# Kernel tuning notes

Hardware: AMD Instinct MI355X
Metric: run time of the kernel (lower is better)

Reference implementation:

```python
import jax, jax.numpy as jnp
import numpy as np

N = 100000      # nodes
E = 1250000     # edges
DIN = 128       # input_feature_dim
H = 64          # hidden_feature_dim
C = 16          # num_classes
BN_EPS = 1e-5


def _linear_init(key, fin, fout):
    # torch.nn.Linear default: U(-1/sqrt(fin), 1/sqrt(fin)); stored as [fin, fout] for x @ W
    s = 1.0 / np.sqrt(fin)
    kw, kb = jax.random.split(key)
    w = jax.random.uniform(kw, (fin, fout), jnp.float32, -s, s)
    b = jax.random.uniform(kb, (fout,), jnp.float32, -s, s)
    return w, b


def setup_inputs() -> dict:
    key = jax.random.key(0)
    ks = jax.random.split(key, 16)
    inp = {}
    inp["x"] = jax.random.normal(ks[0], (N, DIN), jnp.float32)
    src = jax.random.randint(ks[1], (E,), 0, N)
    dst = jax.random.randint(ks[2], (E,), 0, N)
    inp["edge_index"] = jnp.stack([src, dst]).astype(jnp.int64)
    inp["fc1_w"], inp["fc1_b"] = _linear_init(ks[3], DIN, H)
    dims = [(H, H), (H, H), (H, C)]
    for i, (fi, fo) in enumerate(dims):
        w, b = _linear_init(ks[4 + i], fi, fo)
        inp[f"conv{i}_w"] = w
        inp[f"conv{i}_b"] = b
        inp[f"bn{i}_g"] = jnp.ones((fo,), jnp.float32)
        inp[f"bn{i}_b"] = jnp.zeros((fo,), jnp.float32)
    inp["fc2_w"], inp["fc2_b"] = _linear_init(ks[7], C, C)
    return inp


def gcn_conv(h, w, b, src, dst, n):
    # PyG GCNConv: linear transform, add self-loops, symmetric normalization,
    # scatter-add messages from src into dst, then add bias.
    h = h @ w                                   # [N, out]
    loops = jnp.arange(n)
    s = jnp.concatenate([src, loops])           # [E+N]
    d = jnp.concatenate([dst, loops])
    deg = jax.ops.segment_sum(jnp.ones(s.shape[0], h.dtype), d, num_segments=n)
    dinv = jnp.where(deg > 0, jax.lax.rsqrt(deg), 0.0)
    norm = dinv[s] * dinv[d]                    # [E+N]
    msg = h[s] * norm[:, None]                  # [E+N, out] gather + scale
    out = jax.ops.segment_sum(msg, d, num_segments=n)
    return out + b


def batch_norm(x, gamma, beta):
    # BatchNorm1d in training mode: biased batch statistics over nodes
    mu = x.mean(axis=0)
    var = x.var(axis=0)
    return (x - mu) * jax.lax.rsqrt(var + BN_EPS) * gamma + beta


def reference(x, edge_index, fc1_w, fc1_b,
              conv0_w, conv0_b, bn0_g, bn0_b,
              conv1_w, conv1_b, bn1_g, bn1_b,
              conv2_w, conv2_b, bn2_g, bn2_b,
              fc2_w, fc2_b):
    src, dst = edge_index[0], edge_index[1]
    n = x.shape[0]
    h = jax.nn.relu(x @ fc1_w + fc1_b)
    layers = [(conv0_w, conv0_b, bn0_g, bn0_b),
              (conv1_w, conv1_b, bn1_g, bn1_b),
              (conv2_w, conv2_b, bn2_g, bn2_b)]
    for w, b, g, be in layers:
        h = jax.nn.relu(batch_norm(gcn_conv(h, w, b, src, dst, n), g, be))
    h = h @ fc2_w + fc2_b
    return jax.nn.log_softmax(h, axis=1)
```

## Files before the change

kernel.cpp:

```cpp
#include <hip/hip_runtime.h>

#define BN_EPS 1e-5f

typedef unsigned int uint32;

__device__ __forceinline__ void fma4(float4& a, float s, const float4& w) {
    a.x = fmaf(s, w.x, a.x); a.y = fmaf(s, w.y, a.y);
    a.z = fmaf(s, w.z, a.z); a.w = fmaf(s, w.w, a.w);
}

__device__ __forceinline__ float blo(uint32 p) { return __uint_as_float(p << 16); }
__device__ __forceinline__ float bhi(uint32 p) { return __uint_as_float(p & 0xFFFF0000u); }
__device__ __forceinline__ uint32 f2bf1(float f) {
    uint32 u = __float_as_uint(f);
    return (u + 0x7FFFu + ((u >> 16) & 1u)) >> 16;
}
__device__ __forceinline__ uint32 packbf(float a, float b) { return f2bf1(a) | (f2bf1(b) << 16); }


__global__ __launch_bounds__(256) void k_scan1(const int* __restrict__ deg, int* __restrict__ off,
                                               int* __restrict__ bsum, float* __restrict__ dinv, int n) {
    __shared__ int sh[256];
    int i = blockIdx.x * 256 + threadIdx.x;
    int v = (i < n) ? deg[i] : 0;
    if (i < n) dinv[i] = rsqrtf((float)v + 1.0f);
    sh[threadIdx.x] = v;
    __syncthreads();
    #pragma unroll
    for (int d = 1; d < 256; d <<= 1) {
        int t = (threadIdx.x >= d) ? sh[threadIdx.x - d] : 0;
        __syncthreads();
        sh[threadIdx.x] += t;
        __syncthreads();
    }
    if (i < n) off[i] = sh[threadIdx.x] - v;
    if (threadIdx.x == 255) bsum[blockIdx.x] = sh[255];
}

__global__ __launch_bounds__(512) void k_scan2(int* bsum, int nb) {
    __shared__ int sh[512];
    int v = (threadIdx.x < nb) ? bsum[threadIdx.x] : 0;
    sh[threadIdx.x] = v;
    __syncthreads();
    #pragma unroll
    for (int d = 1; d < 512; d <<= 1) {
        int t = (threadIdx.x >= d) ? sh[threadIdx.x - d] : 0;
        __syncthreads();
        sh[threadIdx.x] += t;
        __syncthreads();
    }
    if (threadIdx.x < nb) bsum[threadIdx.x] = sh[threadIdx.x] - v;
}

__global__ __launch_bounds__(256) void k_scan3(int* __restrict__ off, const int* __restrict__ bsum,
                                               int* __restrict__ cnt, int n, int e) {
    int i = blockIdx.x * 256 + threadIdx.x;
    if (i < n) { off[i] += bsum[blockIdx.x]; cnt[i] = 0; }
    if (i == 0) off[n] = e;
}


__global__ __launch_bounds__(256) void k_fc1_deg(const float* __restrict__ X, const float* __restrict__ W,
                                                 const float* __restrict__ bias, float* __restrict__ Y,
                                                 const int* __restrict__ dst, int* __restrict__ deg,
                                                 int n, int e, int nbLin) {
    constexpr int FIN = 128, FOUT = 64, KC = 64;
    constexpr int TX = FOUT / 4, TY = 256 / TX, RQ = 8, TILE_R = TY * RQ;
    __shared__ float Xs[TILE_R][KC + 4];
    __shared__ float Ws[KC][FOUT + 4];

    const int bid = blockIdx.x;
    const int twice = 2 * nbLin;
    bool isLin; int vid;
    if (bid < twice) { isLin = ((bid & 1) == 0); vid = bid >> 1; }
    else { isLin = false; vid = nbLin + (bid - twice); }

    if (!isLin) {
        const int ndeg = gridDim.x - nbLin;
        for (size_t i = (size_t)vid * 256 + threadIdx.x; i < (size_t)e; i += (size_t)ndeg * 256)
            atomicAdd(&deg[dst[i]], 1);
        return;
    }

    const int tx = threadIdx.x % TX;
    const int ty = threadIdx.x / TX;
    const float4 bb = *(const float4*)(bias + tx * 4);

    for (int r0 = vid * TILE_R; r0 < n; r0 += nbLin * TILE_R) {
        float4 acc[RQ];
        #pragma unroll
        for (int q = 0; q < RQ; ++q) acc[q] = bb;

        for (int kc = 0; kc < FIN; kc += KC) {
            __syncthreads();
            for (int idx = threadIdx.x; idx < TILE_R * (KC / 4); idx += 256) {
                int rr = idx / (KC / 4), k4 = idx % (KC / 4);
                int row = r0 + rr;
                float4 v = make_float4(0.f, 0.f, 0.f, 0.f);
                if (row < n) v = *(const float4*)(X + (size_t)row * FIN + kc + 4 * k4);
                *(float4*)(&Xs[rr][4 * k4]) = v;
            }
            for (int idx = threadIdx.x; idx < KC * (FOUT / 4); idx += 256) {
                int kk = idx / (FOUT / 4), c4 = idx % (FOUT / 4);
                *(float4*)(&Ws[kk][4 * c4]) = *(const float4*)(W + (size_t)(kc + kk) * FOUT + 4 * c4);
            }
            __syncthreads();

            #pragma unroll 4
            for (int k4 = 0; k4 < KC / 4; ++k4) {
                float4 w0 = *(const float4*)(&Ws[4*k4+0][tx*4]);
                float4 w1 = *(const float4*)(&Ws[4*k4+1][tx*4]);
                float4 w2 = *(const float4*)(&Ws[4*k4+2][tx*4]);
                float4 w3 = *(const float4*)(&Ws[4*k4+3][tx*4]);
                #pragma unroll
                for (int q = 0; q < RQ; ++q) {
                    float4 xv = *(const float4*)(&Xs[ty*RQ+q][4*k4]);
                    fma4(acc[q], xv.x, w0);
                    fma4(acc[q], xv.y, w1);
                    fma4(acc[q], xv.z, w2);
                    fma4(acc[q], xv.w, w3);
                }
            }
        }

        #pragma unroll
        for (int q = 0; q < RQ; ++q) {
            int row = r0 + ty * RQ + q;
            if (row < n) {
                float4 v = acc[q];
                v.x = fmaxf(v.x, 0.f); v.y = fmaxf(v.y, 0.f);
                v.z = fmaxf(v.z, 0.f); v.w = fmaxf(v.w, 0.f);
                *(float4*)(Y + (size_t)row * FOUT + tx * 4) = v;
            }
        }
    }
}


__global__ __launch_bounds__(256) void k_conv0_fill(const float* __restrict__ X, const float* __restrict__ W,
                                                    uint2* __restrict__ Yb, const float* __restrict__ dinv,
                                                    const int* __restrict__ src, const int* __restrict__ dst,
                                                    const int* __restrict__ off, int* __restrict__ cnt,
                                                    int* __restrict__ esrc, int n, int e, int nbLin) {
    constexpr int FIN = 64, FOUT = 64, KC = 64;
    constexpr int TX = FOUT / 4, TY = 256 / TX, RQ = 8, TILE_R = TY * RQ;
    __shared__ float Xs[TILE_R][KC + 4];
    __shared__ float Ws[KC][FOUT + 4];

    const int bid = blockIdx.x;
    const int twice = 2 * nbLin;
    bool isLin; int vid;
    if (bid < twice) { isLin = ((bid & 1) == 0); vid = bid >> 1; }
    else { isLin = false; vid = nbLin + (bid - twice); }

    if (!isLin) {
        const int nfl = gridDim.x - nbLin;
        for (size_t i = (size_t)vid * 256 + threadIdx.x; i < (size_t)e; i += (size_t)nfl * 256) {
            int d = dst[i];
            int slot = off[d] + atomicAdd(&cnt[d], 1);
            esrc[slot] = src[i];
        }
        return;
    }

    const int tx = threadIdx.x % TX;
    const int ty = threadIdx.x / TX;

    for (int r0 = vid * TILE_R; r0 < n; r0 += nbLin * TILE_R) {
        float4 acc[RQ];
        #pragma unroll
        for (int q = 0; q < RQ; ++q) acc[q] = make_float4(0.f, 0.f, 0.f, 0.f);

        __syncthreads();
        for (int idx = threadIdx.x; idx < TILE_R * (KC / 4); idx += 256) {
            int rr = idx / (KC / 4), k4 = idx % (KC / 4);
            int row = r0 + rr;
            float4 v = make_float4(0.f, 0.f, 0.f, 0.f);
            if (row < n) v = *(const float4*)(X + (size_t)row * FIN + 4 * k4);
            *(float4*)(&Xs[rr][4 * k4]) = v;
        }
        for (int idx = threadIdx.x; idx < KC * (FOUT / 4); idx += 256) {
            int kk = idx / (FOUT / 4), c4 = idx % (FOUT / 4);
            *(float4*)(&Ws[kk][4 * c4]) = *(const float4*)(W + (size_t)kk * FOUT + 4 * c4);
        }
        __syncthreads();

        #pragma unroll 4
        for (int k4 = 0; k4 < KC / 4; ++k4) {
            float4 w0 = *(const float4*)(&Ws[4*k4+0][tx*4]);
            float4 w1 = *(const float4*)(&Ws[4*k4+1][tx*4]);
            float4 w2 = *(const float4*)(&Ws[4*k4+2][tx*4]);
            float4 w3 = *(const float4*)(&Ws[4*k4+3][tx*4]);
            #pragma unroll
            for (int q = 0; q < RQ; ++q) {
                float4 xv = *(const float4*)(&Xs[ty*RQ+q][4*k4]);
                fma4(acc[q], xv.x, w0);
                fma4(acc[q], xv.y, w1);
                fma4(acc[q], xv.z, w2);
                fma4(acc[q], xv.w, w3);
            }
        }

        #pragma unroll
        for (int q = 0; q < RQ; ++q) {
            int row = r0 + ty * RQ + q;
            if (row < n) {
                float4 v = acc[q];
                float dv = dinv[row];
                v.x *= dv; v.y *= dv; v.z *= dv; v.w *= dv;
                uint2 pk;
                pk.x = packbf(v.x, v.y);
                pk.y = packbf(v.z, v.w);
                Yb[(size_t)row * (FOUT / 4) + tx] = pk;
            }
        }
    }
}


template<int FIN, int FOUT, bool RELU, bool BIAS, bool BNIN, bool DSCALE, bool OBF>
__global__ __launch_bounds__(256) void k_linear(const float* __restrict__ X, const float* __restrict__ W,
                                                const float* __restrict__ bias, void* __restrict__ Yv,
                                                const float* __restrict__ S, const float* __restrict__ bng,
                                                const float* __restrict__ bnb, const float* __restrict__ dinv,
                                                float inv_n, int n) {
    constexpr int KC = 64;
    constexpr int TX = FOUT / 4;
    constexpr int TY = 256 / TX;
    constexpr int RQ = (FOUT == 64) ? 8 : 2;
    constexpr int TILE_R = TY * RQ;
    constexpr int LDX = KC + 4;
    constexpr int LDW = FOUT + 4;
    __shared__ float Xs[TILE_R][LDX];
    __shared__ float Ws[KC][LDW];
    __shared__ float scs[BNIN ? FIN : 4], sfs[BNIN ? FIN : 4];

    const int tx = threadIdx.x % TX;
    const int ty = threadIdx.x / TX;

    if (BNIN) {
        for (int c = threadIdx.x; c < FIN; c += 256) {
            float mu = S[c] * inv_n;
            float var = S[FIN + c] * inv_n - mu * mu;
            float is = rsqrtf(var + BN_EPS) * bng[c];
            scs[c] = is;
            sfs[c] = bnb[c] - mu * is;
        }
        __syncthreads();
    }

    float4 bb = make_float4(0.f, 0.f, 0.f, 0.f);
    if (BIAS) bb = *(const float4*)(bias + tx * 4);

    for (int r0 = blockIdx.x * TILE_R; r0 < n; r0 += gridDim.x * TILE_R) {
        float4 acc[RQ];
        #pragma unroll
        for (int q = 0; q < RQ; ++q) acc[q] = bb;

        for (int kc = 0; kc < FIN; kc += KC) {
            __syncthreads();
            for (int idx = threadIdx.x; idx < TILE_R * (KC / 4); idx += 256) {
                int rr = idx / (KC / 4), k4 = idx % (KC / 4);
                int row = r0 + rr;
                float4 v = make_float4(0.f, 0.f, 0.f, 0.f);
                if (row < n) v = *(const float4*)(X + (size_t)row * FIN + kc + 4 * k4);
                if (BNIN) {
                    int c = kc + 4 * k4;
                    v.x = fmaxf(fmaf(v.x, scs[c+0], sfs[c+0]), 0.f);
                    v.y = fmaxf(fmaf(v.y, scs[c+1], sfs[c+1]), 0.f);
                    v.z = fmaxf(fmaf(v.z, scs[c+2], sfs[c+2]), 0.f);
                    v.w = fmaxf(fmaf(v.w, scs[c+3], sfs[c+3]), 0.f);
                }
                *(float4*)(&Xs[rr][4 * k4]) = v;
            }
            for (int idx = threadIdx.x; idx < KC * (FOUT / 4); idx += 256) {
                int kk = idx / (FOUT / 4), c4 = idx % (FOUT / 4);
                *(float4*)(&Ws[kk][4 * c4]) = *(const float4*)(W + (size_t)(kc + kk) * FOUT + 4 * c4);
            }
            __syncthreads();

            #pragma unroll 4
            for (int k4 = 0; k4 < KC / 4; ++k4) {
                float4 w0 = *(const float4*)(&Ws[4*k4+0][tx*4]);
                float4 w1 = *(const float4*)(&Ws[4*k4+1][tx*4]);
                float4 w2 = *(const float4*)(&Ws[4*k4+2][tx*4]);
                float4 w3 = *(const float4*)(&Ws[4*k4+3][tx*4]);
                #pragma unroll
                for (int q = 0; q < RQ; ++q) {
                    float4 xv = *(const float4*)(&Xs[ty*RQ+q][4*k4]);
                    fma4(acc[q], xv.x, w0);
                    fma4(acc[q], xv.y, w1);
                    fma4(acc[q], xv.z, w2);
                    fma4(acc[q], xv.w, w3);
                }
            }
        }

        #pragma unroll
        for (int q = 0; q < RQ; ++q) {
            int row = r0 + ty * RQ + q;
            if (row < n) {
                float4 v = acc[q];
                if (RELU) {
                    v.x = fmaxf(v.x, 0.f); v.y = fmaxf(v.y, 0.f);
                    v.z = fmaxf(v.z, 0.f); v.w = fmaxf(v.w, 0.f);
                }
                if (DSCALE) {
                    float dv = dinv[row];
                    v.x *= dv; v.y *= dv; v.z *= dv; v.w *= dv;
                }
                if (OBF) {
                    uint2 pk;
                    pk.x = packbf(v.x, v.y);
                    pk.y = packbf(v.z, v.w);
                    ((uint2*)Yv)[(size_t)row * (FOUT / 4) + tx] = pk;
                } else {
                    *(float4*)((float*)Yv + (size_t)row * FOUT + tx * 4) = v;
                }
            }
        }
    }
}


__global__ __launch_bounds__(256) void k_accum64bf(const uint32* __restrict__ Tb, const int* __restrict__ esrc,
                                                   const int* __restrict__ off, const float* __restrict__ dinv,
                                                   const float* __restrict__ bias, float* __restrict__ Z,
                                                   float* __restrict__ S, int n, int e) {
    __shared__ uint32 ring[4][2][256];
    __shared__ float sA[4][64], sB[4][64];

    const int lane = threadIdx.x & 63;
    const int wid  = threadIdx.x >> 6;
    const int rsub = lane >> 3;
    const int csub = lane & 7;
    const int cidx = lane >> 1;
    const int chal = lane & 1;
    const float bcol = bias[lane];

    float s1 = 0.f, s2 = 0.f;

    const int gw = blockIdx.x * 4 + wid;
    const int NW = gridDim.x * 4;
    const int eS = (int)((long long)gw * e / NW);
    const int eE = (int)((long long)(gw + 1) * e / NW);

    int lo = 0, hi = n;
    while (lo < hi) { int mid = (lo + hi) >> 1; if (off[mid] < eS) lo = mid + 1; else hi = mid; }
    const int d0 = lo;
    int d1;
    if (gw == NW - 1) d1 = n;
    else {
        lo = d0; hi = n;
        while (lo < hi) { int mid = (lo + hi) >> 1; if (off[mid] < eE) lo = mid + 1; else hi = mid; }
        d1 = lo;
    }

    if (d0 < d1) {
        const int e0 = off[d0];
        const int e1 = off[d1];
        const int nt = (e1 - e0 + 7) >> 3;

        uint32* slot0 = &ring[wid][0][0];
        uint32* slot1 = &ring[wid][1][0];

        int d = d0;
        int nxt = off[d + 1];
        uint32 selfp = Tb[(size_t)d * 32 + cidx];
        float  dv    = dinv[d];
        float  part  = 0.f;
        int    ec    = e0;

        auto tload = [&](int t) -> uint4 {
            int ei = min(e0 + t * 8 + rsub, e1 - 1);
            int s = esrc[ei];
            return ((const uint4*)Tb)[(size_t)s * 8 + csub];
        };

        uint4 B0, B1, B2;
        if (nt > 0) B0 = tload(0);
        if (nt > 1) B1 = tload(1);
        if (nt > 2) B2 = tload(2);

        for (int t = 0; t < nt; ++t) {
            uint32* sl = (t & 1) ? slot1 : slot0;
            uint4 cur = (t % 3 == 0) ? B0 : (t % 3 == 1) ? B1 : B2;
            *(uint4*)(sl + lane * 4) = cur;
            if (t + 3 < nt) {
                if (t % 3 == 0) B0 = tload(t + 3);
                else if (t % 3 == 1) B1 = tload(t + 3);
                else B2 = tload(t + 3);
            }
            int rend = min(8, e1 - (e0 + t * 8));
            for (int r = 0; r < rend; ++r) {
                while (ec == nxt) {
                    float sv = chal ? bhi(selfp) : blo(selfp);
                    float z = fmaf(part + sv, dv, bcol);
                    Z[(size_t)d * 64 + lane] = z;
                    s1 += z; s2 += z * z;
                    part = 0.f;
                    ++d;
                    nxt = off[d + 1];
                    selfp = Tb[(size_t)d * 32 + cidx];
                    dv = dinv[d];
                }
                uint32 p = sl[r * 32 + cidx];
                part += chal ? bhi(p) : blo(p);
                ++ec;
            }
        }
        while (d < d1) {
            float sv = chal ? bhi(selfp) : blo(selfp);
            float z = fmaf(part + sv, dv, bcol);
            Z[(size_t)d * 64 + lane] = z;
            s1 += z; s2 += z * z;
            part = 0.f;
            ++d;
            if (d < d1) {
                selfp = Tb[(size_t)d * 32 + cidx];
                dv = dinv[d];
            }
        }
    }

    sA[wid][lane] = s1;
    sB[wid][lane] = s2;
    __syncthreads();
    if (threadIdx.x < 64) {
        float t1 = 0.f, t2 = 0.f;
        #pragma unroll
        for (int w = 0; w < 4; ++w) { t1 += sA[w][threadIdx.x]; t2 += sB[w][threadIdx.x]; }
        atomicAdd(&S[threadIdx.x], t1);
        atomicAdd(&S[64 + threadIdx.x], t2);
    }
}


__global__ __launch_bounds__(256) void k_accum16bf(const uint2* __restrict__ Tb2, const int* __restrict__ esrc,
                                                   const int* __restrict__ off, const float* __restrict__ dinv,
                                                   const float* __restrict__ bias, float* __restrict__ Z,
                                                   float* __restrict__ S, int n) {
    const int lane = threadIdx.x & 63;
    const int wid  = threadIdx.x >> 6;
    const int lp   = lane & 3;
    const int es   = lane >> 2;
    const float4 bb = *(const float4*)(bias + 4 * lp);
    float st1[4] = {0.f,0.f,0.f,0.f}, st2[4] = {0.f,0.f,0.f,0.f};
    const uint2 z2 = make_uint2(0u, 0u);

    for (int dp = blockIdx.x * 4 + wid; 2 * dp < n; dp += gridDim.x * 4) {
        const int dA = 2 * dp, dB = 2 * dp + 1;
        const int oA0 = off[dA], oA1 = off[dA + 1];
        const int oB0 = oA1;
        const int oB1 = (dB < n) ? off[dB + 1] : oA1;

        float aA0=0.f, aA1=0.f, aA2=0.f, aA3=0.f;
        float aB0=0.f, aB1=0.f, aB2=0.f, aB3=0.f;
        int bA = oA0, bB = oB0;
        while (bA < oA1 || bB < oB1) {
            if (bA < oA1) {
                int i0 = bA + es;
                int s0 = (i0 < oA1) ? esrc[i0] : -1;
                uint2 p0 = (s0 >= 0) ? Tb2[(size_t)s0 * 4 + lp] : z2;
                aA0 += blo(p0.x); aA1 += bhi(p0.x); aA2 += blo(p0.y); aA3 += bhi(p0.y);
            }
            if (bB < oB1) {
                int i0 = bB + es;
                int s0 = (i0 < oB1) ? esrc[i0] : -1;
                uint2 p0 = (s0 >= 0) ? Tb2[(size_t)s0 * 4 + lp] : z2;
                aB0 += blo(p0.x); aB1 += bhi(p0.x); aB2 += blo(p0.y); aB3 += bhi(p0.y);
            }
            bA += 16; bB += 16;
        }

        #pragma unroll
        for (int sh = 4; sh <= 32; sh <<= 1) {
            aA0 += __shfl_xor(aA0, sh); aA1 += __shfl_xor(aA1, sh);
            aA2 += __shfl_xor(aA2, sh); aA3 += __shfl_xor(aA3, sh);
            aB0 += __shfl_xor(aB0, sh); aB1 += __shfl_xor(aB1, sh);
            aB2 += __shfl_xor(aB2, sh); aB3 += __shfl_xor(aB3, sh);
        }

        if (es == 0) {
            uint2 ps = Tb2[(size_t)dA * 4 + lp];
            float dv = dinv[dA];
            float4 zz;
            zz.x = fmaf(aA0 + blo(ps.x), dv, bb.x);
            zz.y = fmaf(aA1 + bhi(ps.x), dv, bb.y);
            zz.z = fmaf(aA2 + blo(ps.y), dv, bb.z);
            zz.w = fmaf(aA3 + bhi(ps.y), dv, bb.w);
            *(float4*)(Z + (size_t)dA * 16 + 4 * lp) = zz;
            st1[0] += zz.x; st2[0] += zz.x * zz.x;
            st1[1] += zz.y; st2[1] += zz.y * zz.y;
            st1[2] += zz.z; st2[2] += zz.z * zz.z;
            st1[3] += zz.w; st2[3] += zz.w * zz.w;
            if (dB < n) {
                uint2 pb = Tb2[(size_t)dB * 4 + lp];
                float dvB = dinv[dB];
                float4 zb;
                zb.x = fmaf(aB0 + blo(pb.x), dvB, bb.x);
                zb.y = fmaf(aB1 + bhi(pb.x), dvB, bb.y);
                zb.z = fmaf(aB2 + blo(pb.y), dvB, bb.z);
                zb.w = fmaf(aB3 + bhi(pb.y), dvB, bb.w);
                *(float4*)(Z + (size_t)dB * 16 + 4 * lp) = zb;
                st1[0] += zb.x; st2[0] += zb.x * zb.x;
                st1[1] += zb.y; st2[1] += zb.y * zb.y;
                st1[2] += zb.z; st2[2] += zb.z * zb.z;
                st1[3] += zb.w; st2[3] += zb.w * zb.w;
            }
        }
    }

    __shared__ float sh1[4][16], sh2[4][16];
    if (es == 0) {
        *(float4*)(&sh1[wid][4 * lp]) = make_float4(st1[0], st1[1], st1[2], st1[3]);
        *(float4*)(&sh2[wid][4 * lp]) = make_float4(st2[0], st2[1], st2[2], st2[3]);
    }
    __syncthreads();
    if (threadIdx.x < 16) {
        float t1 = 0.f, t2 = 0.f;
        #pragma unroll
        for (int w = 0; w < 4; ++w) { t1 += sh1[w][threadIdx.x]; t2 += sh2[w][threadIdx.x]; }
        atomicAdd(&S[threadIdx.x], t1);
        atomicAdd(&S[16 + threadIdx.x], t2);
    }
}


__global__ __launch_bounds__(256) void k_fc2_lsm(const float* __restrict__ Hin, const float* __restrict__ W,
                                                 const float* __restrict__ bias, const float* __restrict__ S,
                                                 const float* __restrict__ bng, const float* __restrict__ bnb,
                                                 float inv_n, float* __restrict__ out, int n) {
    __shared__ float Ws[256];
    __shared__ float bs[16], sc[16], sf[16];
    Ws[threadIdx.x] = W[threadIdx.x];
    if (threadIdx.x < 16) {
        int c = threadIdx.x;
        bs[c] = bias[c];
        float mu = S[c] * inv_n;
        float var = S[16 + c] * inv_n - mu * mu;
        float is = rsqrtf(var + BN_EPS) * bng[c];
        sc[c] = is;
        sf[c] = bnb[c] - mu * is;
    }
    __syncthreads();
    for (int row = blockIdx.x * 256 + threadIdx.x; row < n; row += gridDim.x * 256) {
        float h[16];
        const float4* hp = (const float4*)(Hin + (size_t)row * 16);
        #pragma unroll
        for (int q = 0; q < 4; ++q) {
            float4 h4 = hp[q];
            h[q*4+0] = h4.x; h[q*4+1] = h4.y; h[q*4+2] = h4.z; h[q*4+3] = h4.w;
        }
        #pragma unroll
        for (int k = 0; k < 16; ++k) h[k] = fmaxf(fmaf(h[k], sc[k], sf[k]), 0.0f);
        float o[16];
        #pragma unroll
        for (int c = 0; c < 16; ++c) {
            float acc = bs[c];
            #pragma unroll
            for (int k = 0; k < 16; ++k) acc += h[k] * Ws[k * 16 + c];
            o[c] = acc;
        }
        float m = o[0];
        #pragma unroll
        for (int c = 1; c < 16; ++c) m = fmaxf(m, o[c]);
        float ssum = 0.f;
        #pragma unroll
        for (int c = 0; c < 16; ++c) ssum += expf(o[c] - m);
        float lse = m + logf(ssum);
        float4* op = (float4*)(out + (size_t)row * 16);
        #pragma unroll
        for (int q = 0; q < 4; ++q) {
            float4 w4;
            w4.x = o[q*4+0] - lse; w4.y = o[q*4+1] - lse;
            w4.z = o[q*4+2] - lse; w4.w = o[q*4+3] - lse;
            op[q] = w4;
        }
    }
}


extern "C" void kernel_launch(void* const* d_in, const int* in_sizes, int n_in,
                              void* d_out, int out_size, void* d_ws, size_t ws_size,
                              hipStream_t stream) {
    const float* x      = (const float*)d_in[0];
    const int*   ei     = (const int*)d_in[1];
    const float* fc1_w  = (const float*)d_in[2];
    const float* fc1_b  = (const float*)d_in[3];
    const float* conv_w[3] = { (const float*)d_in[4],  (const float*)d_in[8],  (const float*)d_in[12] };
    const float* conv_b[3] = { (const float*)d_in[5],  (const float*)d_in[9],  (const float*)d_in[13] };
    const float* bn_g[3]   = { (const float*)d_in[6],  (const float*)d_in[10], (const float*)d_in[14] };
    const float* bn_b[3]   = { (const float*)d_in[7],  (const float*)d_in[11], (const float*)d_in[15] };
    const float* fc2_w  = (const float*)d_in[16];
    const float* fc2_b  = (const float*)d_in[17];

    const int n = in_sizes[0] / 128;
    const int e = in_sizes[1] / 2;
    const int* src = ei;
    const int* dst = ei + e;
    const float inv_n = 1.0f / (float)n;

    float*  A    = (float*)d_ws;
    float*  Bf   = A + (size_t)n * 64;
    uint32* Bb   = (uint32*)Bf;
    uint2*  Bb2  = (uint2*)Bf;
    float*  dinv = Bf + (size_t)n * 64;
    int*    deg  = (int*)(dinv + n);
    float*  stats = (float*)(deg + n);
    int*    off  = (int*)(stats + 384);
    int*    esrc = off + n + 1;
    int*    bsum = esrc + e;

    const int gN  = (n + 255) / 256;
    const int gAcc = 2048;
    const int gLin = (n + 127) / 128;
    const int nbLin = gLin;
    const int gFused = 2048;

    float* st[3] = { stats, stats + 128, stats + 256 };

    hipMemsetAsync(deg, 0, ((size_t)n + 384) * sizeof(int), stream);

    k_fc1_deg<<<gFused, 256, 0, stream>>>(x, fc1_w, fc1_b, A, dst, deg, n, e, nbLin);

    k_scan1<<<gN, 256, 0, stream>>>(deg, off, bsum, dinv, n);
    k_scan2<<<1, 512, 0, stream>>>(bsum, gN);
    k_scan3<<<gN, 256, 0, stream>>>(off, bsum, deg , n, e);

    k_conv0_fill<<<gFused, 256, 0, stream>>>(A, conv_w[0], Bb2, dinv, src, dst, off, deg , esrc, n, e, nbLin);
    k_accum64bf<<<gAcc, 256, 0, stream>>>(Bb, esrc, off, dinv, conv_b[0], A, st[0], n, e);

    k_linear<64, 64, false, false, true, true, true><<<gLin, 256, 0, stream>>>(
        A, conv_w[1], nullptr, Bb, st[0], bn_g[0], bn_b[0], dinv, inv_n, n);
    k_accum64bf<<<gAcc, 256, 0, stream>>>(Bb, esrc, off, dinv, conv_b[1], A, st[1], n, e);

    k_linear<64, 16, false, false, true, true, true><<<gLin, 256, 0, stream>>>(
        A, conv_w[2], nullptr, Bb2, st[1], bn_g[1], bn_b[1], dinv, inv_n, n);
    k_accum16bf<<<gAcc, 256, 0, stream>>>(Bb2, esrc, off, dinv, conv_b[2], A, st[2], n);

    k_fc2_lsm<<<gLin, 256, 0, stream>>>(A, fc2_w, fc2_b, st[2], bn_g[2], bn_b[2], inv_n, (float*)d_out, n);
}
```

Measured before the change: 403.8 us.

## Store bf16 hidden features in 16-column chunks and aggregate one chunk per pass

The 64-wide bf16 transformed features are now written in four column-major chunks of 16 columns, so each chunk occupies a contiguous array. The aggregation kernel loops over the four chunks, and each pass gathers 32 edges per tile with two lanes per edge. Partial sums are combined across lane groups with shuffles. The aim is to shrink the gather working set per pass so it stays in cache and to read the edge list with non-temporal loads. The cost is reading the edge list and offsets four times and doing extra shuffle reductions per node.

```diff
diff --git a/kernel.cpp b/kernel.cpp
--- a/kernel.cpp
+++ b/kernel.cpp
@@ -165,6 +165,7 @@
 
     const int tx = threadIdx.x % TX;
     const int ty = threadIdx.x / TX;
+    const int cq = tx >> 2, cr = tx & 3;
 
     for (int r0 = vid * TILE_R; r0 < n; r0 += nbLin * TILE_R) {
         float4 acc[RQ];
@@ -211,7 +212,7 @@
                 uint2 pk;
                 pk.x = packbf(v.x, v.y);
                 pk.y = packbf(v.z, v.w);
-                Yb[(size_t)row * (FOUT / 4) + tx] = pk;
+                Yb[(size_t)cq * n * 4 + (size_t)row * 4 + cr] = pk;
             }
         }
     }
@@ -229,10 +230,8 @@
     constexpr int TY = 256 / TX;
     constexpr int RQ = (FOUT == 64) ? 8 : 2;
     constexpr int TILE_R = TY * RQ;
-    constexpr int LDX = KC + 4;
-    constexpr int LDW = FOUT + 4;
-    __shared__ float Xs[TILE_R][LDX];
-    __shared__ float Ws[KC][LDW];
+    __shared__ float Xs[TILE_R][KC + 4];
+    __shared__ float Ws[KC][FOUT + 4];
     __shared__ float scs[BNIN ? FIN : 4], sfs[BNIN ? FIN : 4];
 
     const int tx = threadIdx.x % TX;
@@ -313,7 +312,12 @@
                     uint2 pk;
                     pk.x = packbf(v.x, v.y);
                     pk.y = packbf(v.z, v.w);
-                    ((uint2*)Yv)[(size_t)row * (FOUT / 4) + tx] = pk;
+                    if (FOUT == 64) {
+                        int cq = tx >> 2, cr = tx & 3;
+                        ((uint2*)Yv)[(size_t)cq * n * 4 + (size_t)row * 4 + cr] = pk;
+                    } else {
+                        ((uint2*)Yv)[(size_t)row * (FOUT / 4) + tx] = pk;
+                    }
                 } else {
                     *(float4*)((float*)Yv + (size_t)row * FOUT + tx * 4) = v;
                 }
@@ -332,13 +336,15 @@
 
     const int lane = threadIdx.x & 63;
     const int wid  = threadIdx.x >> 6;
-    const int rsub = lane >> 3;
-    const int csub = lane & 7;
-    const int cidx = lane >> 1;
-    const int chal = lane & 1;
-    const float bcol = bias[lane];
-
-    float s1 = 0.f, s2 = 0.f;
+    const int sb   = lane >> 4;
+    const int c    = lane & 15;
+    const int cu   = c >> 1;
+    const int ch   = c & 1;
+    const int ge   = lane >> 1;
+    const int gh   = lane & 1;
+
+    sA[wid][lane] = 0.f;
+    sB[wid][lane] = 0.f;
 
     const int gw = blockIdx.x * 4 + wid;
     const int NW = gridDim.x * 4;
@@ -359,72 +365,85 @@
     if (d0 < d1) {
         const int e0 = off[d0];
         const int e1 = off[d1];
-        const int nt = (e1 - e0 + 7) >> 3;
-
+        const int nt = (e1 - e0 + 31) >> 5;
         uint32* slot0 = &ring[wid][0][0];
         uint32* slot1 = &ring[wid][1][0];
 
-        int d = d0;
-        int nxt = off[d + 1];
-        uint32 selfp = Tb[(size_t)d * 32 + cidx];
-        float  dv    = dinv[d];
-        float  part  = 0.f;
-        int    ec    = e0;
-
-        auto tload = [&](int t) -> uint4 {
-            int ei = min(e0 + t * 8 + rsub, e1 - 1);
-            int s = esrc[ei];
-            return ((const uint4*)Tb)[(size_t)s * 8 + csub];
-        };
-
-        uint4 B0, B1, B2;
-        if (nt > 0) B0 = tload(0);
-        if (nt > 1) B1 = tload(1);
-        if (nt > 2) B2 = tload(2);
-
-        for (int t = 0; t < nt; ++t) {
-            uint32* sl = (t & 1) ? slot1 : slot0;
-            uint4 cur = (t % 3 == 0) ? B0 : (t % 3 == 1) ? B1 : B2;
-            *(uint4*)(sl + lane * 4) = cur;
-            if (t + 3 < nt) {
-                if (t % 3 == 0) B0 = tload(t + 3);
-                else if (t % 3 == 1) B1 = tload(t + 3);
-                else B2 = tload(t + 3);
-            }
-            int rend = min(8, e1 - (e0 + t * 8));
-            for (int r = 0; r < rend; ++r) {
-                while (ec == nxt) {
-                    float sv = chal ? bhi(selfp) : blo(selfp);
+        for (int p = 0; p < 4; ++p) {
+            const uint32* chunk  = Tb + (size_t)p * n * 8;
+            const uint4*  chunk4 = (const uint4*)chunk;
+            const float bcol = bias[p * 16 + c];
+            float s1p = 0.f, s2p = 0.f;
+
+            int d = d0;
+            int nxt = off[d + 1];
+            uint32 selfw = chunk[(size_t)d * 8 + cu];
+            float dv = dinv[d];
+            float part = 0.f;
+            int ec = e0;
+
+            auto tload = [&](int t) -> uint4 {
+                int ei = min(e0 + t * 32 + ge, e1 - 1);
+                int sn = __builtin_nontemporal_load(esrc + ei);
+                return chunk4[(size_t)sn * 2 + gh];
+            };
+
+            uint4 B0, B1, B2;
+            if (nt > 0) B0 = tload(0);
+            if (nt > 1) B1 = tload(1);
+            if (nt > 2) B2 = tload(2);
+
+            for (int t = 0; t < nt; ++t) {
+                uint32* sl = (t & 1) ? slot1 : slot0;
+                uint4 cur = (t % 3 == 0) ? B0 : (t % 3 == 1) ? B1 : B2;
+                *(uint4*)(sl + lane * 4) = cur;
+                if (t + 3 < nt) {
+                    if (t % 3 == 0) B0 = tload(t + 3);
+                    else if (t % 3 == 1) B1 = tload(t + 3);
+                    else B2 = tload(t + 3);
+                }
+                const int te0 = e0 + t * 32;
+                const int te1 = min(te0 + 32, e1);
+                while (ec < te1) {
+                    int nend = min(nxt, te1);
+                    for (int j = ec + sb; j < nend; j += 4) {
+                        uint32 pw = sl[(j - te0) * 8 + cu];
+                        part += ch ? bhi(pw) : blo(pw);
+                    }
+                    ec = nend;
+                    if (ec == nxt) {
+                        part += __shfl_xor(part, 16);
+                        part += __shfl_xor(part, 32);
+                        if (sb == 0) {
+                            float sv = ch ? bhi(selfw) : blo(selfw);
+                            float z = fmaf(part + sv, dv, bcol);
+                            __builtin_nontemporal_store(z, Z + (size_t)d * 64 + p * 16 + c);
+                            s1p += z; s2p += z * z;
+                        }
+                        ++d;
+                        if (d < n) { nxt = off[d + 1]; selfw = chunk[(size_t)d * 8 + cu]; dv = dinv[d]; }
+                        else nxt = e + 1;
+                        part = 0.f;
+                    }
+                }
+            }
+            while (d < d1) {
+                part += __shfl_xor(part, 16);
+                part += __shfl_xor(part, 32);
+                if (sb == 0) {
+                    float sv = ch ? bhi(selfw) : blo(selfw);
                     float z = fmaf(part + sv, dv, bcol);
-                    Z[(size_t)d * 64 + lane] = z;
-                    s1 += z; s2 += z * z;
-                    part = 0.f;
-                    ++d;
-                    nxt = off[d + 1];
-                    selfp = Tb[(size_t)d * 32 + cidx];
-                    dv = dinv[d];
-                }
-                uint32 p = sl[r * 32 + cidx];
-                part += chal ? bhi(p) : blo(p);
-                ++ec;
-            }
-        }
-        while (d < d1) {
-            float sv = chal ? bhi(selfp) : blo(selfp);
-            float z = fmaf(part + sv, dv, bcol);
-            Z[(size_t)d * 64 + lane] = z;
-            s1 += z; s2 += z * z;
-            part = 0.f;
-            ++d;
-            if (d < d1) {
-                selfp = Tb[(size_t)d * 32 + cidx];
-                dv = dinv[d];
-            }
-        }
-    }
-
-    sA[wid][lane] = s1;
-    sB[wid][lane] = s2;
+                    __builtin_nontemporal_store(z, Z + (size_t)d * 64 + p * 16 + c);
+                    s1p += z; s2p += z * z;
+                }
+                ++d;
+                if (d < d1) { selfw = chunk[(size_t)d * 8 + cu]; dv = dinv[d]; }
+                part = 0.f;
+            }
+            if (sb == 0) { sA[wid][p * 16 + c] = s1p; sB[wid][p * 16 + c] = s2p; }
+        }
+    }
+
     __syncthreads();
     if (threadIdx.x < 64) {
         float t1 = 0.f, t2 = 0.f;
```

After: 531.7 us. +31.7%, slower.
